# Kernel tuning notes

Hardware: AMD Instinct MI355X
Metric: run time of the kernel (lower is better)

Reference implementation:

```python
import jax, jax.numpy as jnp
import numpy as np

D, FH, FW = 41, 16, 44          # depth bins (arange(4,45,1)), feat H/W = 256/16, 704/16
NX, NY, NZ = 128, 128, 1        # BEV grid from grid_conf
C_CTX = 64                      # LSS context channels
EPS = 1e-5


def _frustum():
    ds = jnp.arange(4.0, 45.0, 1.0)                 # (D,)
    xs = jnp.linspace(0.0, 703.0, FW)
    ys = jnp.linspace(0.0, 255.0, FH)
    return jnp.stack([
        jnp.broadcast_to(xs[None, None, :], (D, FH, FW)),
        jnp.broadcast_to(ys[None, :, None], (D, FH, FW)),
        jnp.broadcast_to(ds[:, None, None], (D, FH, FW)),
    ], -1)                                           # (D,FH,FW,3)


def _bn(x, g, b, m, v):
    # inference-mode BatchNorm2d, x: (B,C,H,W)
    scale = g / jnp.sqrt(v + EPS)
    return x * scale[None, :, None, None] + (b - m * scale)[None, :, None, None]


def setup_inputs() -> dict:
    key = jax.random.key(0)
    ks = jax.random.split(key, 24)
    B, N = 4, 6
    imgs = jax.random.normal(ks[0], (B, N, 3, 256, 704), jnp.float32)
    eye = jnp.eye(3, dtype=jnp.float32)
    # well-conditioned camera matrices (code takes torch.inverse of these)
    rots = eye + 0.05 * jax.random.normal(ks[1], (B, N, 3, 3), jnp.float32)
    trans = 2.0 * jax.random.normal(ks[2], (B, N, 3), jnp.float32)
    K = jnp.array([[500., 0., 352.], [0., 500., 128.], [0., 0., 1.]], jnp.float32)
    kmask = jnp.array([[1., 0., 1.], [0., 1., 1.], [0., 0., 0.]], jnp.float32)
    intrins = K + 5.0 * jax.random.normal(ks[3], (B, N, 3, 3), jnp.float32) * kmask
    post_rots = eye + 0.01 * jax.random.normal(ks[4], (B, N, 3, 3), jnp.float32)
    post_trans = jax.random.normal(ks[5], (B, N, 3), jnp.float32)
    # backbone: Conv2d(3,256,16,16) + BN(256)
    conv_w = 0.02 * jax.random.normal(ks[6], (256, 3, 16, 16), jnp.float32)
    conv_b = 0.01 * jax.random.normal(ks[7], (256,), jnp.float32)
    bn1_g = 1.0 + 0.1 * jax.random.normal(ks[8], (256,), jnp.float32)
    bn1_b = 0.1 * jax.random.normal(ks[9], (256,), jnp.float32)
    bn1_m = 0.1 * jax.random.normal(ks[10], (256,), jnp.float32)
    bn1_v = jax.random.uniform(ks[11], (256,), jnp.float32, 0.5, 1.5)
    # depth_net: Conv2d(256, D+64=105, 1)
    depth_w = 0.05 * jax.random.normal(ks[12], (D + C_CTX, 256), jnp.float32)
    depth_b = 0.01 * jax.random.normal(ks[13], (D + C_CTX,), jnp.float32)
    # BEV encoder: Conv2d(128,64,3,pad=1) + BN(64)
    enc_w = 0.05 * jax.random.normal(ks[14], (64, 128, 3, 3), jnp.float32)
    enc_b = 0.01 * jax.random.normal(ks[15], (64,), jnp.float32)
    bn2_g = 1.0 + 0.1 * jax.random.normal(ks[16], (64,), jnp.float32)
    bn2_b = 0.1 * jax.random.normal(ks[17], (64,), jnp.float32)
    bn2_m = 0.1 * jax.random.normal(ks[18], (64,), jnp.float32)
    bn2_v = jax.random.uniform(ks[19], (64,), jnp.float32, 0.5, 1.5)
    # head: Conv2d(64, 7, 1)
    head_w = 0.05 * jax.random.normal(ks[20], (7, 64), jnp.float32)
    head_b = 0.01 * jax.random.normal(ks[21], (7,), jnp.float32)
    return dict(curr_imgs=imgs, rots=rots, trans=trans, intrins=intrins,
                post_rots=post_rots, post_trans=post_trans,
                conv_w=conv_w, conv_b=conv_b, bn1_g=bn1_g, bn1_b=bn1_b,
                bn1_m=bn1_m, bn1_v=bn1_v, depth_w=depth_w, depth_b=depth_b,
                enc_w=enc_w, enc_b=enc_b, bn2_g=bn2_g, bn2_b=bn2_b,
                bn2_m=bn2_m, bn2_v=bn2_v, head_w=head_w, head_b=head_b)


def _forward(curr_imgs, rots, trans, intrins, post_rots, post_trans,
             conv_w, conv_b, bn1_g, bn1_b, bn1_m, bn1_v,
             depth_w, depth_b, enc_w, enc_b, bn2_g, bn2_b, bn2_m, bn2_v,
             head_w, head_b):
    B, N = curr_imgs.shape[:2]
    dn = ('NCHW', 'OIHW', 'NCHW')
    # backbone (patchify conv + BN + ReLU)
    x = curr_imgs.reshape(B * N, 3, 256, 704)
    x = jax.lax.conv_general_dilated(x, conv_w, (16, 16), 'VALID', dimension_numbers=dn)
    x = jax.nn.relu(_bn(x + conv_b[None, :, None, None], bn1_g, bn1_b, bn1_m, bn1_v))  # (BN,256,16,44)
    # depth net (1x1 conv) -> depth softmax + context
    y = jnp.einsum('oc,bchw->bohw', depth_w, x) + depth_b[None, :, None, None]
    depth = jax.nn.softmax(y[:, :D], axis=1)                 # (BN,D,H,W)
    ctx = y[:, D:]                                           # (BN,C,H,W)
    # LSS outer product: (BN,C,D,H,W) -> (B,N,D,H,W,C)
    outer = ctx[:, :, None] * depth[:, None]
    outer = outer.reshape(B, N, C_CTX, D, FH, FW).transpose(0, 1, 3, 4, 5, 2)
    # geometry: pixel frustum -> ego coords
    fr = _frustum()                                          # (D,FH,FW,3)
    pts = fr[None, None] - post_trans[:, :, None, None, None, :]
    pts = jnp.einsum('bnij,bndhwj->bndhwi', jnp.linalg.inv(post_rots), pts)
    pts = jnp.concatenate([pts[..., :2] * pts[..., 2:3], pts[..., 2:3]], -1)
    comb = rots @ jnp.linalg.inv(intrins)
    pts = jnp.einsum('bnij,bndhwj->bndhwi', comb, pts) + trans[:, :, None, None, None, :]
    # voxel pooling (segment-sum == sort+cumsum trick of the original)
    dx = jnp.array([0.8, 0.8, 20.0], jnp.float32)
    low = jnp.array([-51.2, -51.2, -10.0], jnp.float32)      # bx - dx/2
    coords = ((pts.reshape(-1, 3) - low) / dx).astype(jnp.int32)  # trunc-to-zero like .long()
    rank = coords[:, 0] + coords[:, 1] * NX + coords[:, 2] * NX * NY
    tot = NX * NY * NZ
    kept = (rank >= 0) & (rank < tot)                        # combined-rank check only (as in source)
    feats = outer.reshape(-1, C_CTX) * kept[:, None].astype(outer.dtype)
    bev_flat = jax.ops.segment_sum(feats, jnp.where(kept, rank, 0), num_segments=tot)
    bev = bev_flat.reshape(NZ, NY, NX, C_CTX).transpose(0, 3, 1, 2)  # (1,64,128,128); batch mixed as in source
    # temporal fusion (prev_bev=None branch): cat(bev, bev)
    feat = jnp.concatenate([bev, bev], 1)                    # (1,128,128,128)
    feat = jax.lax.conv_general_dilated(feat, enc_w, (1, 1), 'SAME', dimension_numbers=dn)
    feat = jax.nn.relu(_bn(feat + enc_b[None, :, None, None], bn2_g, bn2_b, bn2_m, bn2_v))
    out = jnp.einsum('oc,bchw->bohw', head_w, feat) + head_b[None, :, None, None]
    return out, bev


def reference(curr_imgs, rots, trans, intrins, post_rots, post_trans,
              conv_w, conv_b, bn1_g, bn1_b, bn1_m, bn1_v,
              depth_w, depth_b, enc_w, enc_b, bn2_g, bn2_b, bn2_m, bn2_v,
              head_w, head_b):
    return _forward(curr_imgs, rots, trans, intrins, post_rots, post_trans,
                    conv_w, conv_b, bn1_g, bn1_b, bn1_m, bn1_v,
                    depth_w, depth_b, enc_w, enc_b, bn2_g, bn2_b, bn2_m, bn2_v,
                    head_w, head_b)
```

## Files before the change

kernel.cpp:

```cpp
#include <hip/hip_runtime.h>
#include <hip/hip_bf16.h>
#include <hip/hip_fp16.h>

#define NPTS 692736
#define NPATCH 16896

typedef _Float16 h16;
typedef __attribute__((ext_vector_type(4))) _Float16 half4v;
typedef __attribute__((ext_vector_type(8))) _Float16 half8v;
typedef __attribute__((ext_vector_type(4))) float f32x4;

__device__ float  v11_xbuf[NPATCH*256];
__device__ float  v11_ctx[NPATCH*64];
__device__ float  v11_depth[NPATCH*41];
__device__ int    v11_ranks[NPTS];
__device__ float  v11_bev[16384*64];
__device__ double v11_geom[24*24];

__device__ h16    v20_whi[196608];
__device__ h16    v20_wlo[196608];

__device__ h16    v15_dwhi[112*256];
__device__ h16    v15_dwlo[112*256];

__device__ h16    v16_w2hi[64*576];
__device__ h16    v16_w2lo[64*576];

__device__ int    v12_cnt[16384];
__device__ int    v12_off[16384];
__device__ int    v12_pos[NPTS];
__device__ int2   v12_sorted[NPTS];
__device__ int    v12_total;

__device__ __forceinline__ void inv3_v11(const double* m, double* o){
  double a=m[0],b=m[1],c=m[2],d=m[3],e=m[4],f=m[5],g=m[6],h=m[7],i=m[8];
  double A = e*i - f*h, B = -(d*i - f*g), C = d*h - e*g;
  double det = a*A + b*B + c*C;
  double id = 1.0/det;
  o[0]=A*id;            o[1]=-(b*i - c*h)*id; o[2]=(b*f - c*e)*id;
  o[3]=B*id;            o[4]=(a*i - c*g)*id;  o[5]=-(a*f - c*d)*id;
  o[6]=C*id;            o[7]=-(a*h - b*g)*id; o[8]=(a*e - b*d)*id;
}

__global__ void prep_v20(const float* cw, const float* dw, const float* enc_w,
                         const float* rots, const float* trans, const float* intrins,
                         const float* post_rots, const float* post_trans){
  int b = blockIdx.x;
  int tid = threadIdx.x;
  if (b < 4096){
    int gid = b*256 + tid;
    v11_bev[gid] = 0.f;
    if (gid < 16384) v12_cnt[gid] = 0;
  } else if (b < 4864){
    int gid = (b-4096)*256 + tid;
    int e  = gid & 7;
    int t  = gid >> 3;
    int o  = t & 63;
    int t2 = t >> 6;
    int kc = t2 & 7;
    int t3 = t2 >> 3;
    int kt = t3 % 12;
    int ob = t3 / 12;
    int k  = kt*64 + kc*8 + e;
    int oc = ob*64 + o;
    float x = cw[oc*768 + k];
    h16 hi = (h16)x;
    v20_whi[gid] = hi;
    v20_wlo[gid] = (h16)(x - (float)hi);
  } else if (b < 4976){
    int gid = (b-4864)*256 + tid;
    int o = gid >> 8, c = gid & 255;
    float x = (o < 105) ? dw[o*256 + c] : 0.f;
    h16 hi = (h16)x;
    v15_dwhi[gid] = hi;
    v15_dwlo[gid] = (h16)(x - (float)hi);
  } else if (b < 5120){
    int gid = (b-4976)*256 + tid;
    if (gid < 36864){
      int o = gid / 576; int k = gid % 576;
      int tap = k >> 6, ic = k & 63;
      float x = enc_w[o*1152 + ic*9 + tap] + enc_w[o*1152 + (ic+64)*9 + tap];
      h16 hi = (h16)x;
      v16_w2hi[gid] = hi;
      v16_w2lo[gid] = (h16)(x - (float)hi);
    }
  } else {
    int t = tid;
    if (t >= 24) return;
    double pr[9], it[9], r[9];
    for (int i=0;i<9;i++){
      pr[i] = (double)post_rots[t*9+i];
      it[i] = (double)intrins[t*9+i];
      r[i]  = (double)rots[t*9+i];
    }
    double ipr[9], iit[9];
    inv3_v11(pr, ipr); inv3_v11(it, iit);
    double* g = v11_geom + t*24;
    for (int i=0;i<3;i++) for(int j=0;j<3;j++){
      double s=0; for(int k=0;k<3;k++) s += r[i*3+k]*iit[k*3+j];
      g[9+i*3+j]=s;
    }
    for (int i=0;i<9;i++) g[i]   = ipr[i];
    for (int i=0;i<3;i++) g[18+i]= (double)post_trans[t*3+i];
    for (int i=0;i<3;i++) g[21+i]= (double)trans[t*3+i];
  }
}

__global__ __launch_bounds__(256) void conv1_v20(const float* img,
    const float* cb, const float* g1, const float* b1, const float* m1, const float* v1){
  __shared__ __align__(16) h16 Ah[8][64][8];
  __shared__ __align__(16) h16 Al[8][64][8];
  __shared__ __align__(16) h16 Bh[4096];
  __shared__ __align__(16) h16 Bl[4096];
  int tid  = threadIdx.x;
  int lane = tid & 63, wv = tid >> 6;
  int wr = wv >> 1, wc = wv & 1;
  int pbase = blockIdx.x * 64;

  int pp0 = tid >> 3, kc0 = tid & 7;
  const float* ab[2];
  #pragma unroll
  for (int i=0;i<2;i++){
    int p = pbase + pp0 + 32*i;
    int im = p/704, pix = p%704;
    int ph = pix/44, pw = pix%44;
    ab[i] = img + (size_t)im*540672 + (size_t)ph*16*704 + pw*16;
  }
  const h16* wph = v20_whi + (size_t)blockIdx.y*12*4096;
  const h16* wpl = v20_wlo + (size_t)blockIdx.y*12*4096;

  float4 pa0[2], pa1[2];
  half8v pbh[2], pbl[2];

  auto LOAD_A = [&](int ktI){
    int k0 = ktI*64 + kc0*8;
    int c = k0>>8, rem = k0&255, ky = rem>>4, kx = rem&15;
    size_t goff = (size_t)c*180224 + ky*704 + kx;
    #pragma unroll
    for (int i=0;i<2;i++){
      pa0[i] = *(const float4*)(ab[i] + goff);
      pa1[i] = *(const float4*)(ab[i] + goff + 4);
    }
  };
  auto LOAD_B = [&](int ktI){
    const h16* ph = wph + (size_t)ktI*4096;
    const h16* pl = wpl + (size_t)ktI*4096;
    #pragma unroll
    for (int i=0;i<2;i++){
      int l = tid + i*256;
      pbh[i] = *(const half8v*)(ph + l*8);
      pbl[i] = *(const half8v*)(pl + l*8);
    }
  };

  f32x4 acc[2][2];
  #pragma unroll
  for (int mf=0;mf<2;mf++)
    #pragma unroll
    for (int nf=0;nf<2;nf++) acc[mf][nf] = (f32x4){0.f,0.f,0.f,0.f};

  int fr = lane & 15, fg = lane >> 4;

  LOAD_A(0); LOAD_B(0);

  for (int ktI=0; ktI<12; ktI++){
    __syncthreads();
    #pragma unroll
    for (int i=0;i<2;i++){
      float vv[8] = {pa0[i].x,pa0[i].y,pa0[i].z,pa0[i].w,
                     pa1[i].x,pa1[i].y,pa1[i].z,pa1[i].w};
      half8v hv, lv;
      #pragma unroll
      for (int e=0;e<8;e++){ h16 h=(h16)vv[e]; hv[e]=h; lv[e]=(h16)(vv[e]-(float)h); }
      int srow = (pp0 + 32*i) ^ kc0;
      *(half8v*)&Ah[kc0][srow][0] = hv;
      *(half8v*)&Al[kc0][srow][0] = lv;
    }
    #pragma unroll
    for (int i=0;i<2;i++){
      int l = tid + i*256;
      *(half8v*)&Bh[l*8] = pbh[i];
      *(half8v*)&Bl[l*8] = pbl[i];
    }
    __syncthreads();
    if (ktI < 11){ LOAD_A(ktI+1); LOAD_B(ktI+1); }
    #pragma unroll
    for (int ks=0;ks<2;ks++){
      int kc = ks*4 + fg;
      half8v ah[2], al[2], bh[2], bl[2];
      #pragma unroll
      for (int mf=0;mf<2;mf++){
        int row = (wr*32 + mf*16 + fr) ^ kc;
        ah[mf] = *(const half8v*)&Ah[kc][row][0];
        al[mf] = *(const half8v*)&Al[kc][row][0];
      }
      #pragma unroll
      for (int nf=0;nf<2;nf++){
        int col = wc*32 + nf*16 + fr;
        bh[nf] = *(const half8v*)&Bh[(kc*64 + col)*8];
        bl[nf] = *(const half8v*)&Bl[(kc*64 + col)*8];
      }
      #pragma unroll
      for (int mf=0;mf<2;mf++)
        #pragma unroll
        for (int nf=0;nf<2;nf++){
          acc[mf][nf] = __builtin_amdgcn_mfma_f32_16x16x32_f16(ah[mf], bh[nf], acc[mf][nf], 0,0,0);
          acc[mf][nf] = __builtin_amdgcn_mfma_f32_16x16x32_f16(ah[mf], bl[nf], acc[mf][nf], 0,0,0);
          acc[mf][nf] = __builtin_amdgcn_mfma_f32_16x16x32_f16(al[mf], bh[nf], acc[mf][nf], 0,0,0);
        }
    }
  }
  int obase = blockIdx.y * 64;
  #pragma unroll
  for (int nf=0;nf<2;nf++){
    int ch = obase + wc*32 + nf*16 + fr;
    float sc = g1[ch] / sqrtf(v1[ch] + 1e-5f);
    float sh = b1[ch] - m1[ch]*sc;
    float bi = cb[ch];
    #pragma unroll
    for (int mf=0;mf<2;mf++){
      #pragma unroll
      for (int j=0;j<4;j++){
        int pq = pbase + wr*32 + mf*16 + fg*4 + j;
        float t = (acc[mf][nf][j] + bi)*sc + sh;
        v11_xbuf[(size_t)pq*256 + ch] = t > 0.f ? t : 0.f;
      }
    }
  }
}

__global__ __launch_bounds__(256) void depth_v16(const float* db){
  __shared__ __align__(16) h16 Ah[4][64][8];
  __shared__ __align__(16) h16 Al[4][64][8];
  __shared__ __align__(16) h16 Bh[4][112][8];
  __shared__ __align__(16) h16 Bl[4][112][8];
  __shared__ float sy[64*113];
  int tid = threadIdx.x;
  int lane = tid & 63, wv = tid >> 6;
  int pbase = blockIdx.x*64;
  int fr = lane & 15, fg = lane >> 4;

  int app = tid & 63;
  int kcA = tid >> 6;
  const float* xsrc = &v11_xbuf[(size_t)(pbase+app)*256 + kcA*8];

  f32x4 acc[7];
  #pragma unroll
  for (int nf=0;nf<7;nf++) acc[nf] = (f32x4){0.f,0.f,0.f,0.f};

  for (int kt=0; kt<256; kt+=32){
    __syncthreads();
    {
      float4 v0 = *(const float4*)(xsrc + kt);
      float4 v1 = *(const float4*)(xsrc + kt + 4);
      float vv[8] = {v0.x,v0.y,v0.z,v0.w,v1.x,v1.y,v1.z,v1.w};
      half8v hv, lv;
      #pragma unroll
      for (int e=0;e<8;e++){ h16 h=(h16)vv[e]; hv[e]=h; lv[e]=(h16)(vv[e]-(float)h); }
      *(half8v*)&Ah[kcA][app][0] = hv;
      *(half8v*)&Al[kcA][app][0] = lv;
    }
    for (int l = tid; l < 448; l += 256){
      int kc = l/112, o = l%112;
      *(half8v*)&Bh[kc][o][0] = *(const half8v*)&v15_dwhi[o*256 + kt + kc*8];
      *(half8v*)&Bl[kc][o][0] = *(const half8v*)&v15_dwlo[o*256 + kt + kc*8];
    }
    __syncthreads();
    int row = wv*16 + fr;
    half8v ah = *(const half8v*)&Ah[fg][row][0];
    half8v al = *(const half8v*)&Al[fg][row][0];
    #pragma unroll
    for (int nf=0;nf<7;nf++){
      int col = nf*16 + fr;
      half8v bh = *(const half8v*)&Bh[fg][col][0];
      half8v bl = *(const half8v*)&Bl[fg][col][0];
      acc[nf] = __builtin_amdgcn_mfma_f32_16x16x32_f16(ah, bh, acc[nf], 0,0,0);
      acc[nf] = __builtin_amdgcn_mfma_f32_16x16x32_f16(ah, bl, acc[nf], 0,0,0);
      acc[nf] = __builtin_amdgcn_mfma_f32_16x16x32_f16(al, bh, acc[nf], 0,0,0);
    }
  }
  #pragma unroll
  for (int nf=0;nf<7;nf++){
    int o = nf*16 + fr;
    if (o < 105){
      float bias = db[o];
      #pragma unroll
      for (int j=0;j<4;j++){
        int pp = wv*16 + fg*4 + j;
        sy[pp*113 + o] = acc[nf][j] + bias;
      }
    }
  }
  __syncthreads();
  if (tid < 64){
    float* y = &sy[tid*113];
    float m = y[0];
    for (int i=1;i<41;i++) m = fmaxf(m, y[i]);
    float s = 0.f;
    for (int i=0;i<41;i++){ float e = expf(y[i]-m); y[i] = e; s += e; }
    float inv = 1.f/s;
    for (int i=0;i<41;i++) y[i] *= inv;
  }
  __syncthreads();
  for (int l = tid; l < 64*41; l += 256){
    int pp = l/41, dd = l%41;
    v11_depth[(size_t)(pbase+pp)*41 + dd] = sy[pp*113+dd];
  }
  for (int l = tid; l < 64*64; l += 256){
    int pp = l>>6, c = l&63;
    v11_ctx[(size_t)(pbase+pp)*64 + c] = sy[pp*113 + 41 + c];
  }
}

__global__ __launch_bounds__(256) void rank_v13(){
  __shared__ int lh[16384];
  int tid = threadIdx.x;
  for (int i = tid; i < 16384; i += 256) lh[i] = 0;
  __syncthreads();
  int base = blockIdx.x*1024;
  int rk[4], lp[4];
  #pragma unroll
  for (int k=0;k<4;k++){
    int idx = base + k*256 + tid;
    rk[k] = -1; lp[k] = 0;
    if (idx < NPTS){
      int im = idx / 28864;
      int r  = idx % 28864;
      int d  = r / 704; int pix = r % 704;
      int h = pix / 44, w = pix % 44;
      const double* g = v11_geom + im*24;
      double fx = (double)w * (703.0/43.0);
      double fy = (double)h * 17.0;
      double fz = 4.0 + (double)d;
      double px = fx - g[18], py = fy - g[19], pz = fz - g[20];
      double q0 = g[0]*px + g[1]*py + g[2]*pz;
      double q1 = g[3]*px + g[4]*py + g[5]*pz;
      double q2 = g[6]*px + g[7]*py + g[8]*pz;
      q0 *= q2; q1 *= q2;
      double o0 = g[9]*q0  + g[10]*q1 + g[11]*q2 + g[21];
      double o1 = g[12]*q0 + g[13]*q1 + g[14]*q2 + g[22];
      double o2 = g[15]*q0 + g[16]*q1 + g[17]*q2 + g[23];
      int cx = (int)((o0 + 51.2)/0.8);
      int cy = (int)((o1 + 51.2)/0.8);
      int cz = (int)((o2 + 10.0)/20.0);
      int rank = cx + cy*128 + cz*16384;
      if (rank >= 0 && rank < 16384){
        rk[k] = rank;
        lp[k] = atomicAdd(&lh[rank], 1);
      }
    }
  }
  __syncthreads();
  for (int i = tid; i < 16384; i += 256){
    int h = lh[i];
    if (h) lh[i] = atomicAdd(&v12_cnt[i], h);
  }
  __syncthreads();
  #pragma unroll
  for (int k=0;k<4;k++){
    int idx = base + k*256 + tid;
    if (idx < NPTS){
      v11_ranks[idx] = rk[k];
      if (rk[k] >= 0) v12_pos[idx] = lh[rk[k]] + lp[k];
    }
  }
}

__global__ __launch_bounds__(256) void scan_v13(){
  __shared__ int part[256];
  int t = threadIdx.x;
  int base = t*64;
  int s = 0;
  for (int i=0;i<64;i++) s += v12_cnt[base+i];
  part[t] = s;
  __syncthreads();
  if (t == 0){
    int run = 0;
    for (int i=0;i<256;i++){ int v = part[i]; part[i] = run; run += v; }
    v12_total = run;
  }
  __syncthreads();
  int run = part[t];
  for (int i=0;i<64;i++){
    v12_off[base+i] = run;
    run += v12_cnt[base+i];
  }
}

__global__ __launch_bounds__(256) void fill_v13(){
  int idx = blockIdx.x*256 + threadIdx.x;
  if (idx >= NPTS) return;
  int rank = v11_ranks[idx];
  if (rank < 0) return;
  int im = idx / 28864;
  int r  = idx % 28864;
  int d  = r / 704; int pix = r % 704;
  int p  = im*704 + pix;
  int pos = v12_off[rank] + v12_pos[idx];
  v12_sorted[pos] = make_int2((p<<6) | d, rank);
}

__global__ __launch_bounds__(256) void gather_v13(){
  int total = v12_total;
  int w = threadIdx.x >> 6;
  int chunk = blockIdx.x*256 + w*64;
  if (chunk >= total) return;
  int lane = threadIdx.x & 63;
  int n = total - chunk; if (n > 64) n = 64;
  int pv = 0, rv = -1;
  float dv = 0.f;
  if (lane < n){
    int2 sr = v12_sorted[chunk + lane];
    pv = sr.x; rv = sr.y;
    dv = v11_depth[(pv>>6)*41 + (pv & 63)];
  }
  float acc = 0.f;
  int cur = __shfl(rv, 0);
  for (int i = 0; i < n; i++){
    int rk = __shfl(rv, i);
    int pp = __shfl(pv, i) >> 6;
    float dd = __shfl(dv, i);
    if (rk != cur){
      atomicAdd(&v11_bev[(size_t)cur*64 + lane], acc);
      acc = 0.f; cur = rk;
    }
    acc += v11_ctx[(pp<<6) | lane] * dd;
  }
  atomicAdd(&v11_bev[(size_t)cur*64 + lane], acc);
}

__global__ void bevout_v11(float* out1){
  int gid = blockIdx.x*256 + threadIdx.x;
  int c  = gid >> 14;
  int yx = gid & 16383;
  out1[gid] = v11_bev[(size_t)yx*64 + c];
}

__global__ __launch_bounds__(256) void conv2_v17(
    const float* eb, const float* g2, const float* b2_, const float* m2, const float* v2,
    const float* hw, const float* hb, float* out0){
  __shared__ __align__(16) h16 Ah[4][64][8];
  __shared__ __align__(16) h16 Al[4][64][8];
  __shared__ __align__(16) h16 Bh[4][64][8];
  __shared__ __align__(16) h16 Bl[4][64][8];
  __shared__ float sfeat[64*68];
  __shared__ float hred[4*64*7];
  int tid = threadIdx.x;
  int lane = tid & 63, wv = tid >> 6;
  int bx = blockIdx.x & 15, by = blockIdx.x >> 4;
  int fr = lane & 15, fg = lane >> 4;

  int app = tid & 63;
  int kcT = tid >> 6;
  int apy = app >> 3, apx = app & 7;

  f32x4 acc[4];
  #pragma unroll
  for (int nf=0;nf<4;nf++) acc[nf] = (f32x4){0.f,0.f,0.f,0.f};

  for (int kt=0; kt<576; kt+=32){
    int tap = kt >> 6, ic0 = kt & 32;
    int dy = tap/3 - 1, dx = tap%3 - 1;
    __syncthreads();
    {
      int gy = by*8 + apy + dy, gx = bx*8 + apx + dx;
      float4 v0 = {0.f,0.f,0.f,0.f}, v1 = {0.f,0.f,0.f,0.f};
      if (gy>=0 && gy<128 && gx>=0 && gx<128){
        const float* src = &v11_bev[(size_t)(gy*128+gx)*64 + ic0 + kcT*8];
        v0 = *(const float4*)src;
        v1 = *(const float4*)(src+4);
      }
      float vv[8] = {v0.x,v0.y,v0.z,v0.w,v1.x,v1.y,v1.z,v1.w};
      half8v hv, lv;
      #pragma unroll
      for (int e=0;e<8;e++){ h16 h=(h16)vv[e]; hv[e]=h; lv[e]=(h16)(vv[e]-(float)h); }
      *(half8v*)&Ah[kcT][app][0] = hv;
      *(half8v*)&Al[kcT][app][0] = lv;
    }
    {
      *(half8v*)&Bh[kcT][app][0] = *(const half8v*)&v16_w2hi[app*576 + kt + kcT*8];
      *(half8v*)&Bl[kcT][app][0] = *(const half8v*)&v16_w2lo[app*576 + kt + kcT*8];
    }
    __syncthreads();
    int row = wv*16 + fr;
    half8v ah = *(const half8v*)&Ah[fg][row][0];
    half8v al = *(const half8v*)&Al[fg][row][0];
    #pragma unroll
    for (int nf=0;nf<4;nf++){
      int col = nf*16 + fr;
      half8v bh = *(const half8v*)&Bh[fg][col][0];
      half8v bl = *(const half8v*)&Bl[fg][col][0];
      acc[nf] = __builtin_amdgcn_mfma_f32_16x16x32_f16(ah, bh, acc[nf], 0,0,0);
      acc[nf] = __builtin_amdgcn_mfma_f32_16x16x32_f16(ah, bl, acc[nf], 0,0,0);
      acc[nf] = __builtin_amdgcn_mfma_f32_16x16x32_f16(al, bh, acc[nf], 0,0,0);
    }
  }
  #pragma unroll
  for (int nf=0;nf<4;nf++){
    int ch = nf*16 + fr;
    float sc = g2[ch]/sqrtf(v2[ch]+1e-5f);
    float sh = b2_[ch] - m2[ch]*sc;
    float bi = eb[ch];
    #pragma unroll
    for (int j=0;j<4;j++){
      int pp = wv*16 + fg*4 + j;
      float t = (acc[nf][j] + bi)*sc + sh;
      sfeat[pp*68 + ch] = t > 0.f ? t : 0.f;
    }
  }
  __syncthreads();
  int og = tid >> 6, pix = tid & 63;
  float part[7];
  #pragma unroll
  for (int o=0;o<7;o++) part[o]=0.f;
  #pragma unroll
  for (int j=0;j<16;j++){
    int oc = og*16 + j;
    float v = sfeat[pix*68 + oc];
    #pragma unroll
    for (int o=0;o<7;o++) part[o] += hw[o*64+oc]*v;
  }
  #pragma unroll
  for (int o=0;o<7;o++) hred[(og*64+pix)*7+o] = part[o];
  __syncthreads();
  if (og == 0){
    int gy = by*8 + (pix>>3), gx = bx*8 + (pix&7);
    #pragma unroll
    for (int o=0;o<7;o++){
      float s = hred[pix*7+o] + hred[(64+pix)*7+o] + hred[(128+pix)*7+o]
              + hred[(192+pix)*7+o] + hb[o];
      out0[o*16384 + gy*128 + gx] = s;
    }
  }
}

extern "C" void kernel_launch(void* const* d_in, const int* in_sizes, int n_in,
                              void* d_out, int out_size, void* d_ws, size_t ws_size,
                              hipStream_t stream){
  const float* imgs       = (const float*)d_in[0];
  const float* rots       = (const float*)d_in[1];
  const float* trans      = (const float*)d_in[2];
  const float* intrins    = (const float*)d_in[3];
  const float* post_rots  = (const float*)d_in[4];
  const float* post_trans = (const float*)d_in[5];
  const float* conv_w     = (const float*)d_in[6];
  const float* conv_b     = (const float*)d_in[7];
  const float* bn1_g      = (const float*)d_in[8];
  const float* bn1_b      = (const float*)d_in[9];
  const float* bn1_m      = (const float*)d_in[10];
  const float* bn1_v      = (const float*)d_in[11];
  const float* depth_w    = (const float*)d_in[12];
  const float* depth_b    = (const float*)d_in[13];
  const float* enc_w      = (const float*)d_in[14];
  const float* enc_b      = (const float*)d_in[15];
  const float* bn2_g      = (const float*)d_in[16];
  const float* bn2_b      = (const float*)d_in[17];
  const float* bn2_m      = (const float*)d_in[18];
  const float* bn2_v      = (const float*)d_in[19];
  const float* head_w     = (const float*)d_in[20];
  const float* head_b     = (const float*)d_in[21];

  float* out0 = (float*)d_out;
  float* out1 = out0 + 114688;

  prep_v20<<<5121, 256, 0, stream>>>(conv_w, depth_w, enc_w,
                                     rots, trans, intrins, post_rots, post_trans);
  conv1_v20<<<dim3(264, 4), 256, 0, stream>>>(imgs, conv_b, bn1_g, bn1_b, bn1_m, bn1_v);
  depth_v16<<<264, 256, 0, stream>>>(depth_b);
  rank_v13<<<(NPTS+1023)/1024, 256, 0, stream>>>();
  scan_v13<<<1, 256, 0, stream>>>();
  fill_v13<<<NPTS/256, 256, 0, stream>>>();
  gather_v13<<<NPTS/256, 256, 0, stream>>>();
  bevout_v11<<<4096, 256, 0, stream>>>(out1);
  conv2_v17<<<256, 256, 0, stream>>>(enc_b, bn2_g, bn2_b, bn2_m, bn2_v,
                                     head_w, head_b, out0);
}
```

Measured before the change: 260.4 us.

## Pre-swizzle weights into MFMA fragment order, read directly, fuse BEV transpose into conv2

Weights for conv1, depth and conv2 are now pre-laid out in prep in per-lane MFMA fragment order. Each lane loads its B operand straight from global memory, so the shared-memory staging of weights and its stores are gone. conv1 uses a 1D grid remapped so that consecutive blocks on the same XCD share pixel tiles across output blocks. The separate bevout transpose kernel is removed: conv2 writes out1 during its center-tap load, saving one launch and one pass over the BEV buffer. The cost is repeated global/L2 reads of the weights per wave instead of one shared copy per block.

```diff
diff --git a/kernel.cpp b/kernel.cpp
--- a/kernel.cpp
+++ b/kernel.cpp
@@ -17,14 +17,14 @@
 __device__ float  v11_bev[16384*64];
 __device__ double v11_geom[24*24];
 
-__device__ h16    v20_whi[196608];
-__device__ h16    v20_wlo[196608];
-
-__device__ h16    v15_dwhi[112*256];
-__device__ h16    v15_dwlo[112*256];
-
-__device__ h16    v16_w2hi[64*576];
-__device__ h16    v16_w2lo[64*576];
+__device__ h16    v21_whi[196608];
+__device__ h16    v21_wlo[196608];
+
+__device__ h16    v21_dwhi[28672];
+__device__ h16    v21_dwlo[28672];
+
+__device__ h16    v21_w2hi[36864];
+__device__ h16    v21_w2lo[36864];
 
 __device__ int    v12_cnt[16384];
 __device__ int    v12_off[16384];
@@ -42,7 +42,7 @@
   o[6]=C*id;            o[7]=-(a*h - b*g)*id; o[8]=(a*e - b*d)*id;
 }
 
-__global__ void prep_v20(const float* cw, const float* dw, const float* enc_w,
+__global__ void prep_v21(const float* cw, const float* dw, const float* enc_w,
                          const float* rots, const float* trans, const float* intrins,
                          const float* post_rots, const float* post_trans){
   int b = blockIdx.x;
@@ -54,35 +54,48 @@
   } else if (b < 4864){
     int gid = (b-4096)*256 + tid;
     int e  = gid & 7;
-    int t  = gid >> 3;
-    int o  = t & 63;
-    int t2 = t >> 6;
-    int kc = t2 & 7;
-    int t3 = t2 >> 3;
-    int kt = t3 % 12;
-    int ob = t3 / 12;
-    int k  = kt*64 + kc*8 + e;
-    int oc = ob*64 + o;
+    int fr = (gid>>3) & 15;
+    int fg = (gid>>7) & 3;
+    int ks = (gid>>9) & 1;
+    int og = (gid>>10) & 3;
+    int rest = gid >> 12;
+    int kt = rest % 12;
+    int ob = rest / 12;
+    int k  = kt*64 + ks*32 + fg*8 + e;
+    int oc = ob*64 + og*16 + fr;
     float x = cw[oc*768 + k];
     h16 hi = (h16)x;
-    v20_whi[gid] = hi;
-    v20_wlo[gid] = (h16)(x - (float)hi);
+    v21_whi[gid] = hi;
+    v21_wlo[gid] = (h16)(x - (float)hi);
   } else if (b < 4976){
     int gid = (b-4864)*256 + tid;
-    int o = gid >> 8, c = gid & 255;
+    int e   = gid & 7;
+    int fr  = (gid>>3) & 15;
+    int fg  = (gid>>7) & 3;
+    int ktI = (gid>>9) & 7;
+    int nf  = gid >> 12;
+    int o = nf*16 + fr;
+    int c = ktI*32 + fg*8 + e;
     float x = (o < 105) ? dw[o*256 + c] : 0.f;
     h16 hi = (h16)x;
-    v15_dwhi[gid] = hi;
-    v15_dwlo[gid] = (h16)(x - (float)hi);
+    v21_dwhi[gid] = hi;
+    v21_dwlo[gid] = (h16)(x - (float)hi);
   } else if (b < 5120){
     int gid = (b-4976)*256 + tid;
     if (gid < 36864){
-      int o = gid / 576; int k = gid % 576;
+      int e  = gid & 7;
+      int fr = (gid>>3) & 15;
+      int fg = (gid>>7) & 3;
+      int t  = gid >> 9;
+      int ktI = t % 18;
+      int nf  = t / 18;
+      int o = nf*16 + fr;
+      int k = ktI*32 + fg*8 + e;
       int tap = k >> 6, ic = k & 63;
       float x = enc_w[o*1152 + ic*9 + tap] + enc_w[o*1152 + (ic+64)*9 + tap];
       h16 hi = (h16)x;
-      v16_w2hi[gid] = hi;
-      v16_w2lo[gid] = (h16)(x - (float)hi);
+      v21_w2hi[gid] = hi;
+      v21_w2lo[gid] = (h16)(x - (float)hi);
     }
   } else {
     int t = tid;
@@ -106,16 +119,19 @@
   }
 }
 
-__global__ __launch_bounds__(256) void conv1_v20(const float* img,
+__global__ __launch_bounds__(256) void conv1_v21(const float* img,
     const float* cb, const float* g1, const float* b1, const float* m1, const float* v1){
   __shared__ __align__(16) h16 Ah[8][64][8];
   __shared__ __align__(16) h16 Al[8][64][8];
-  __shared__ __align__(16) h16 Bh[4096];
-  __shared__ __align__(16) h16 Bl[4096];
   int tid  = threadIdx.x;
   int lane = tid & 63, wv = tid >> 6;
   int wr = wv >> 1, wc = wv & 1;
-  int pbase = blockIdx.x * 64;
+  int bid = blockIdx.x;
+  int xcd = bid & 7;
+  int s   = bid >> 3;
+  int ob  = s & 3;
+  int pb  = (s >> 2) + 33*xcd;
+  int pbase = pb * 64;
 
   int pp0 = tid >> 3, kc0 = tid & 7;
   const float* ab[2];
@@ -126,12 +142,8 @@
     int ph = pix/44, pw = pix%44;
     ab[i] = img + (size_t)im*540672 + (size_t)ph*16*704 + pw*16;
   }
-  const h16* wph = v20_whi + (size_t)blockIdx.y*12*4096;
-  const h16* wpl = v20_wlo + (size_t)blockIdx.y*12*4096;
 
   float4 pa0[2], pa1[2];
-  half8v pbh[2], pbl[2];
-
   auto LOAD_A = [&](int ktI){
     int k0 = ktI*64 + kc0*8;
     int c = k0>>8, rem = k0&255, ky = rem>>4, kx = rem&15;
@@ -142,16 +154,6 @@
       pa1[i] = *(const float4*)(ab[i] + goff + 4);
     }
   };
-  auto LOAD_B = [&](int ktI){
-    const h16* ph = wph + (size_t)ktI*4096;
-    const h16* pl = wpl + (size_t)ktI*4096;
-    #pragma unroll
-    for (int i=0;i<2;i++){
-      int l = tid + i*256;
-      pbh[i] = *(const half8v*)(ph + l*8);
-      pbl[i] = *(const half8v*)(pl + l*8);
-    }
-  };
 
   f32x4 acc[2][2];
   #pragma unroll
@@ -160,8 +162,9 @@
     for (int nf=0;nf<2;nf++) acc[mf][nf] = (f32x4){0.f,0.f,0.f,0.f};
 
   int fr = lane & 15, fg = lane >> 4;
-
-  LOAD_A(0); LOAD_B(0);
+  int lo8 = lane*8;
+
+  LOAD_A(0);
 
   for (int ktI=0; ktI<12; ktI++){
     __syncthreads();
@@ -176,18 +179,13 @@
       *(half8v*)&Ah[kc0][srow][0] = hv;
       *(half8v*)&Al[kc0][srow][0] = lv;
     }
-    #pragma unroll
-    for (int i=0;i<2;i++){
-      int l = tid + i*256;
-      *(half8v*)&Bh[l*8] = pbh[i];
-      *(half8v*)&Bl[l*8] = pbl[i];
-    }
     __syncthreads();
-    if (ktI < 11){ LOAD_A(ktI+1); LOAD_B(ktI+1); }
+    if (ktI < 11) LOAD_A(ktI+1);
+    int btile = (ob*12 + ktI) << 12;
     #pragma unroll
     for (int ks=0;ks<2;ks++){
       int kc = ks*4 + fg;
-      half8v ah[2], al[2], bh[2], bl[2];
+      half8v ah[2], al[2];
       #pragma unroll
       for (int mf=0;mf<2;mf++){
         int row = (wr*32 + mf*16 + fr) ^ kc;
@@ -196,21 +194,20 @@
       }
       #pragma unroll
       for (int nf=0;nf<2;nf++){
-        int col = wc*32 + nf*16 + fr;
-        bh[nf] = *(const half8v*)&Bh[(kc*64 + col)*8];
-        bl[nf] = *(const half8v*)&Bl[(kc*64 + col)*8];
-      }
-      #pragma unroll
-      for (int mf=0;mf<2;mf++)
+        int og = wc*2 + nf;
+        int bidx = btile + ((og*2 + ks) << 9) + lo8;
+        half8v bh = *(const half8v*)&v21_whi[bidx];
+        half8v bl = *(const half8v*)&v21_wlo[bidx];
         #pragma unroll
-        for (int nf=0;nf<2;nf++){
-          acc[mf][nf] = __builtin_amdgcn_mfma_f32_16x16x32_f16(ah[mf], bh[nf], acc[mf][nf], 0,0,0);
-          acc[mf][nf] = __builtin_amdgcn_mfma_f32_16x16x32_f16(ah[mf], bl[nf], acc[mf][nf], 0,0,0);
-          acc[mf][nf] = __builtin_amdgcn_mfma_f32_16x16x32_f16(al[mf], bh[nf], acc[mf][nf], 0,0,0);
+        for (int mf=0;mf<2;mf++){
+          acc[mf][nf] = __builtin_amdgcn_mfma_f32_16x16x32_f16(ah[mf], bh, acc[mf][nf], 0,0,0);
+          acc[mf][nf] = __builtin_amdgcn_mfma_f32_16x16x32_f16(ah[mf], bl, acc[mf][nf], 0,0,0);
+          acc[mf][nf] = __builtin_amdgcn_mfma_f32_16x16x32_f16(al[mf], bh, acc[mf][nf], 0,0,0);
         }
-    }
-  }
-  int obase = blockIdx.y * 64;
+      }
+    }
+  }
+  int obase = ob * 64;
   #pragma unroll
   for (int nf=0;nf<2;nf++){
     int ch = obase + wc*32 + nf*16 + fr;
@@ -229,16 +226,15 @@
   }
 }
 
-__global__ __launch_bounds__(256) void depth_v16(const float* db){
+__global__ __launch_bounds__(256) void depth_v18(const float* db){
   __shared__ __align__(16) h16 Ah[4][64][8];
   __shared__ __align__(16) h16 Al[4][64][8];
-  __shared__ __align__(16) h16 Bh[4][112][8];
-  __shared__ __align__(16) h16 Bl[4][112][8];
   __shared__ float sy[64*113];
   int tid = threadIdx.x;
   int lane = tid & 63, wv = tid >> 6;
   int pbase = blockIdx.x*64;
   int fr = lane & 15, fg = lane >> 4;
+  int lo8 = lane*8;
 
   int app = tid & 63;
   int kcA = tid >> 6;
@@ -248,22 +244,17 @@
   #pragma unroll
   for (int nf=0;nf<7;nf++) acc[nf] = (f32x4){0.f,0.f,0.f,0.f};
 
-  for (int kt=0; kt<256; kt+=32){
+  for (int ktI=0; ktI<8; ktI++){
     __syncthreads();
     {
-      float4 v0 = *(const float4*)(xsrc + kt);
-      float4 v1 = *(const float4*)(xsrc + kt + 4);
+      float4 v0 = *(const float4*)(xsrc + ktI*32);
+      float4 v1 = *(const float4*)(xsrc + ktI*32 + 4);
       float vv[8] = {v0.x,v0.y,v0.z,v0.w,v1.x,v1.y,v1.z,v1.w};
       half8v hv, lv;
       #pragma unroll
       for (int e=0;e<8;e++){ h16 h=(h16)vv[e]; hv[e]=h; lv[e]=(h16)(vv[e]-(float)h); }
       *(half8v*)&Ah[kcA][app][0] = hv;
       *(half8v*)&Al[kcA][app][0] = lv;
-    }
-    for (int l = tid; l < 448; l += 256){
-      int kc = l/112, o = l%112;
-      *(half8v*)&Bh[kc][o][0] = *(const half8v*)&v15_dwhi[o*256 + kt + kc*8];
-      *(half8v*)&Bl[kc][o][0] = *(const half8v*)&v15_dwlo[o*256 + kt + kc*8];
     }
     __syncthreads();
     int row = wv*16 + fr;
@@ -271,9 +262,9 @@
     half8v al = *(const half8v*)&Al[fg][row][0];
     #pragma unroll
     for (int nf=0;nf<7;nf++){
-      int col = nf*16 + fr;
-      half8v bh = *(const half8v*)&Bh[fg][col][0];
-      half8v bl = *(const half8v*)&Bl[fg][col][0];
+      int bidx = ((nf*8 + ktI) << 9) + lo8;
+      half8v bh = *(const half8v*)&v21_dwhi[bidx];
+      half8v bl = *(const half8v*)&v21_dwlo[bidx];
       acc[nf] = __builtin_amdgcn_mfma_f32_16x16x32_f16(ah, bh, acc[nf], 0,0,0);
       acc[nf] = __builtin_amdgcn_mfma_f32_16x16x32_f16(ah, bl, acc[nf], 0,0,0);
       acc[nf] = __builtin_amdgcn_mfma_f32_16x16x32_f16(al, bh, acc[nf], 0,0,0);
@@ -429,26 +420,18 @@
   atomicAdd(&v11_bev[(size_t)cur*64 + lane], acc);
 }
 
-__global__ void bevout_v11(float* out1){
-  int gid = blockIdx.x*256 + threadIdx.x;
-  int c  = gid >> 14;
-  int yx = gid & 16383;
-  out1[gid] = v11_bev[(size_t)yx*64 + c];
-}
-
-__global__ __launch_bounds__(256) void conv2_v17(
+__global__ __launch_bounds__(256) void conv2_v19(
     const float* eb, const float* g2, const float* b2_, const float* m2, const float* v2,
-    const float* hw, const float* hb, float* out0){
+    const float* hw, const float* hb, float* out0, float* out1){
   __shared__ __align__(16) h16 Ah[4][64][8];
   __shared__ __align__(16) h16 Al[4][64][8];
-  __shared__ __align__(16) h16 Bh[4][64][8];
-  __shared__ __align__(16) h16 Bl[4][64][8];
   __shared__ float sfeat[64*68];
   __shared__ float hred[4*64*7];
   int tid = threadIdx.x;
   int lane = tid & 63, wv = tid >> 6;
   int bx = blockIdx.x & 15, by = blockIdx.x >> 4;
   int fr = lane & 15, fg = lane >> 4;
+  int lo8 = lane*8;
 
   int app = tid & 63;
   int kcT = tid >> 6;
@@ -458,7 +441,8 @@
   #pragma unroll
   for (int nf=0;nf<4;nf++) acc[nf] = (f32x4){0.f,0.f,0.f,0.f};
 
-  for (int kt=0; kt<576; kt+=32){
+  for (int ktI=0; ktI<18; ktI++){
+    int kt = ktI*32;
     int tap = kt >> 6, ic0 = kt & 32;
     int dy = tap/3 - 1, dx = tap%3 - 1;
     __syncthreads();
@@ -471,15 +455,18 @@
         v1 = *(const float4*)(src+4);
       }
       float vv[8] = {v0.x,v0.y,v0.z,v0.w,v1.x,v1.y,v1.z,v1.w};
+      if (tap == 4){
+        int gyc = by*8 + apy, gxc = bx*8 + apx;
+        int ch0 = ic0 + kcT*8;
+        #pragma unroll
+        for (int q=0;q<8;q++)
+          out1[(ch0+q)*16384 + gyc*128 + gxc] = vv[q];
+      }
       half8v hv, lv;
       #pragma unroll
       for (int e=0;e<8;e++){ h16 h=(h16)vv[e]; hv[e]=h; lv[e]=(h16)(vv[e]-(float)h); }
       *(half8v*)&Ah[kcT][app][0] = hv;
       *(half8v*)&Al[kcT][app][0] = lv;
-    }
-    {
-      *(half8v*)&Bh[kcT][app][0] = *(const half8v*)&v16_w2hi[app*576 + kt + kcT*8];
-      *(half8v*)&Bl[kcT][app][0] = *(const half8v*)&v16_w2lo[app*576 + kt + kcT*8];
     }
     __syncthreads();
     int row = wv*16 + fr;
@@ -487,9 +474,9 @@
     half8v al = *(const half8v*)&Al[fg][row][0];
     #pragma unroll
     for (int nf=0;nf<4;nf++){
-      int col = nf*16 + fr;
-      half8v bh = *(const half8v*)&Bh[fg][col][0];
-      half8v bl = *(const half8v*)&Bl[fg][col][0];
+      int bidx = ((nf*18 + ktI) << 9) + lo8;
+      half8v bh = *(const half8v*)&v21_w2hi[bidx];
+      half8v bl = *(const half8v*)&v21_w2lo[bidx];
       acc[nf] = __builtin_amdgcn_mfma_f32_16x16x32_f16(ah, bh, acc[nf], 0,0,0);
       acc[nf] = __builtin_amdgcn_mfma_f32_16x16x32_f16(ah, bl, acc[nf], 0,0,0);
       acc[nf] = __builtin_amdgcn_mfma_f32_16x16x32_f16(al, bh, acc[nf], 0,0,0);
@@ -563,15 +550,14 @@
   float* out0 = (float*)d_out;
   float* out1 = out0 + 114688;
 
-  prep_v20<<<5121, 256, 0, stream>>>(conv_w, depth_w, enc_w,
+  prep_v21<<<5121, 256, 0, stream>>>(conv_w, depth_w, enc_w,
                                      rots, trans, intrins, post_rots, post_trans);
-  conv1_v20<<<dim3(264, 4), 256, 0, stream>>>(imgs, conv_b, bn1_g, bn1_b, bn1_m, bn1_v);
-  depth_v16<<<264, 256, 0, stream>>>(depth_b);
+  conv1_v21<<<1056, 256, 0, stream>>>(imgs, conv_b, bn1_g, bn1_b, bn1_m, bn1_v);
+  depth_v18<<<264, 256, 0, stream>>>(depth_b);
   rank_v13<<<(NPTS+1023)/1024, 256, 0, stream>>>();
   scan_v13<<<1, 256, 0, stream>>>();
   fill_v13<<<NPTS/256, 256, 0, stream>>>();
   gather_v13<<<NPTS/256, 256, 0, stream>>>();
-  bevout_v11<<<4096, 256, 0, stream>>>(out1);
-  conv2_v17<<<256, 256, 0, stream>>>(enc_b, bn2_g, bn2_b, bn2_m, bn2_v,
-                                     head_w, head_b, out0);
-}
+  conv2_v19<<<256, 256, 0, stream>>>(enc_b, bn2_g, bn2_b, bn2_m, bn2_v,
+                                     head_w, head_b, out0, out1);
+}
```

New measurement: 278.5 us. +6.9%, slower.

## Load conv1 weight fragments directly into registers and remap blocks by XCD

Applied to the files above, without the earlier changes.

Weights are re-packed in the prep kernel into an MFMA-fragment-ordered layout so each lane reads its B operands straight from global memory into double-buffered registers. This removes the B shared-memory tiles and their stores and loads. The grid is also flattened to 1D with an XCD-aware mapping, so the four output-channel blocks for the same pixel tile land on the same XCD and can share L2 for image reads. The cost is more registers per thread and redundant weight loads across waves, with no reuse through LDS.

```diff
diff --git a/kernel.cpp b/kernel.cpp
--- a/kernel.cpp
+++ b/kernel.cpp
@@ -17,8 +17,8 @@
 __device__ float  v11_bev[16384*64];
 __device__ double v11_geom[24*24];
 
-__device__ h16    v20_whi[196608];
-__device__ h16    v20_wlo[196608];
+__device__ h16    v21_whi[196608];
+__device__ h16    v21_wlo[196608];
 
 __device__ h16    v15_dwhi[112*256];
 __device__ h16    v15_dwlo[112*256];
@@ -42,7 +42,7 @@
   o[6]=C*id;            o[7]=-(a*h - b*g)*id; o[8]=(a*e - b*d)*id;
 }
 
-__global__ void prep_v20(const float* cw, const float* dw, const float* enc_w,
+__global__ void prep_v22(const float* cw, const float* dw, const float* enc_w,
                          const float* rots, const float* trans, const float* intrins,
                          const float* post_rots, const float* post_trans){
   int b = blockIdx.x;
@@ -54,19 +54,19 @@
   } else if (b < 4864){
     int gid = (b-4096)*256 + tid;
     int e  = gid & 7;
-    int t  = gid >> 3;
-    int o  = t & 63;
-    int t2 = t >> 6;
-    int kc = t2 & 7;
-    int t3 = t2 >> 3;
-    int kt = t3 % 12;
-    int ob = t3 / 12;
-    int k  = kt*64 + kc*8 + e;
-    int oc = ob*64 + o;
+    int fr = (gid>>3) & 15;
+    int fg = (gid>>7) & 3;
+    int ks = (gid>>9) & 1;
+    int og = (gid>>10) & 3;
+    int rest = gid >> 12;
+    int kt = rest % 12;
+    int ob = rest / 12;
+    int k  = kt*64 + ks*32 + fg*8 + e;
+    int oc = ob*64 + og*16 + fr;
     float x = cw[oc*768 + k];
     h16 hi = (h16)x;
-    v20_whi[gid] = hi;
-    v20_wlo[gid] = (h16)(x - (float)hi);
+    v21_whi[gid] = hi;
+    v21_wlo[gid] = (h16)(x - (float)hi);
   } else if (b < 4976){
     int gid = (b-4864)*256 + tid;
     int o = gid >> 8, c = gid & 255;
@@ -106,16 +106,19 @@
   }
 }
 
-__global__ __launch_bounds__(256) void conv1_v20(const float* img,
+__global__ __launch_bounds__(256) void conv1_v22(const float* img,
     const float* cb, const float* g1, const float* b1, const float* m1, const float* v1){
   __shared__ __align__(16) h16 Ah[8][64][8];
   __shared__ __align__(16) h16 Al[8][64][8];
-  __shared__ __align__(16) h16 Bh[4096];
-  __shared__ __align__(16) h16 Bl[4096];
   int tid  = threadIdx.x;
   int lane = tid & 63, wv = tid >> 6;
   int wr = wv >> 1, wc = wv & 1;
-  int pbase = blockIdx.x * 64;
+  int bid = blockIdx.x;
+  int xcd = bid & 7;
+  int s   = bid >> 3;
+  int ob  = s & 3;
+  int pb  = (s >> 2) + 33*xcd;
+  int pbase = pb * 64;
 
   int pp0 = tid >> 3, kc0 = tid & 7;
   const float* ab[2];
@@ -126,11 +129,12 @@
     int ph = pix/44, pw = pix%44;
     ab[i] = img + (size_t)im*540672 + (size_t)ph*16*704 + pw*16;
   }
-  const h16* wph = v20_whi + (size_t)blockIdx.y*12*4096;
-  const h16* wpl = v20_wlo + (size_t)blockIdx.y*12*4096;
+
+  int fr = lane & 15, fg = lane >> 4;
+  int lo8 = lane*8;
 
   float4 pa0[2], pa1[2];
-  half8v pbh[2], pbl[2];
+  half8v pbh[2][4], pbl[2][4];
 
   auto LOAD_A = [&](int ktI){
     int k0 = ktI*64 + kc0*8;
@@ -142,15 +146,17 @@
       pa1[i] = *(const float4*)(ab[i] + goff + 4);
     }
   };
-  auto LOAD_B = [&](int ktI){
-    const h16* ph = wph + (size_t)ktI*4096;
-    const h16* pl = wpl + (size_t)ktI*4096;
-    #pragma unroll
-    for (int i=0;i<2;i++){
-      int l = tid + i*256;
-      pbh[i] = *(const half8v*)(ph + l*8);
-      pbl[i] = *(const half8v*)(pl + l*8);
-    }
+  auto LOAD_B = [&](int ktI, int par){
+    int btile = (ob*12 + ktI) << 12;
+    #pragma unroll
+    for (int ks=0;ks<2;ks++)
+      #pragma unroll
+      for (int nf=0;nf<2;nf++){
+        int og = wc*2 + nf;
+        int bidx = btile + ((og*2 + ks) << 9) + lo8;
+        pbh[par][ks*2+nf] = *(const half8v*)&v21_whi[bidx];
+        pbl[par][ks*2+nf] = *(const half8v*)&v21_wlo[bidx];
+      }
   };
 
   f32x4 acc[2][2];
@@ -159,11 +165,11 @@
     #pragma unroll
     for (int nf=0;nf<2;nf++) acc[mf][nf] = (f32x4){0.f,0.f,0.f,0.f};
 
-  int fr = lane & 15, fg = lane >> 4;
-
-  LOAD_A(0); LOAD_B(0);
-
+  LOAD_A(0); LOAD_B(0, 0);
+
+  #pragma unroll
   for (int ktI=0; ktI<12; ktI++){
+    int par = ktI & 1;
     __syncthreads();
     #pragma unroll
     for (int i=0;i<2;i++){
@@ -176,18 +182,12 @@
       *(half8v*)&Ah[kc0][srow][0] = hv;
       *(half8v*)&Al[kc0][srow][0] = lv;
     }
-    #pragma unroll
-    for (int i=0;i<2;i++){
-      int l = tid + i*256;
-      *(half8v*)&Bh[l*8] = pbh[i];
-      *(half8v*)&Bl[l*8] = pbl[i];
-    }
     __syncthreads();
-    if (ktI < 11){ LOAD_A(ktI+1); LOAD_B(ktI+1); }
+    if (ktI < 11){ LOAD_A(ktI+1); LOAD_B(ktI+1, par^1); }
     #pragma unroll
     for (int ks=0;ks<2;ks++){
       int kc = ks*4 + fg;
-      half8v ah[2], al[2], bh[2], bl[2];
+      half8v ah[2], al[2];
       #pragma unroll
       for (int mf=0;mf<2;mf++){
         int row = (wr*32 + mf*16 + fr) ^ kc;
@@ -196,21 +196,18 @@
       }
       #pragma unroll
       for (int nf=0;nf<2;nf++){
-        int col = wc*32 + nf*16 + fr;
-        bh[nf] = *(const half8v*)&Bh[(kc*64 + col)*8];
-        bl[nf] = *(const half8v*)&Bl[(kc*64 + col)*8];
-      }
-      #pragma unroll
-      for (int mf=0;mf<2;mf++)
+        half8v bh = pbh[par][ks*2+nf];
+        half8v bl = pbl[par][ks*2+nf];
         #pragma unroll
-        for (int nf=0;nf<2;nf++){
-          acc[mf][nf] = __builtin_amdgcn_mfma_f32_16x16x32_f16(ah[mf], bh[nf], acc[mf][nf], 0,0,0);
-          acc[mf][nf] = __builtin_amdgcn_mfma_f32_16x16x32_f16(ah[mf], bl[nf], acc[mf][nf], 0,0,0);
-          acc[mf][nf] = __builtin_amdgcn_mfma_f32_16x16x32_f16(al[mf], bh[nf], acc[mf][nf], 0,0,0);
+        for (int mf=0;mf<2;mf++){
+          acc[mf][nf] = __builtin_amdgcn_mfma_f32_16x16x32_f16(ah[mf], bh, acc[mf][nf], 0,0,0);
+          acc[mf][nf] = __builtin_amdgcn_mfma_f32_16x16x32_f16(ah[mf], bl, acc[mf][nf], 0,0,0);
+          acc[mf][nf] = __builtin_amdgcn_mfma_f32_16x16x32_f16(al[mf], bh, acc[mf][nf], 0,0,0);
         }
-    }
-  }
-  int obase = blockIdx.y * 64;
+      }
+    }
+  }
+  int obase = ob * 64;
   #pragma unroll
   for (int nf=0;nf<2;nf++){
     int ch = obase + wc*32 + nf*16 + fr;
@@ -563,9 +560,9 @@
   float* out0 = (float*)d_out;
   float* out1 = out0 + 114688;
 
-  prep_v20<<<5121, 256, 0, stream>>>(conv_w, depth_w, enc_w,
+  prep_v22<<<5121, 256, 0, stream>>>(conv_w, depth_w, enc_w,
                                      rots, trans, intrins, post_rots, post_trans);
-  conv1_v20<<<dim3(264, 4), 256, 0, stream>>>(imgs, conv_b, bn1_g, bn1_b, bn1_m, bn1_v);
+  conv1_v22<<<1056, 256, 0, stream>>>(imgs, conv_b, bn1_g, bn1_b, bn1_m, bn1_v);
   depth_v16<<<264, 256, 0, stream>>>(depth_b);
   rank_v13<<<(NPTS+1023)/1024, 256, 0, stream>>>();
   scan_v13<<<1, 256, 0, stream>>>();
```

Result: slower. 269.3 us (+3.4%).
